# Optimization experiments

Hardware: AMD Instinct MI355X
Metric: run time of the kernel (lower is better)

## Reference

```python
import jax, jax.numpy as jnp
import numpy as np

N = 100000      # nodes
R = 3           # relations
E = 1600000     # edges per relation
IN, HID, OUT = 128, 128, 64


def setup_inputs() -> dict:
    key = jax.random.key(0)
    ks = jax.random.split(key, 16)
    x = jax.random.normal(ks[0], (N, IN), dtype=jnp.float32)
    src = jax.random.randint(ks[1], (R, E), 0, N, dtype=jnp.int32)
    dst = jax.random.randint(ks[2], (R, E), 0, N, dtype=jnp.int32)
    dims = [(IN, HID), (HID, HID), (HID, HID), (HID, HID), (HID, HID), (HID, OUT)]
    inp = {"x": x, "src": src, "dst": dst}
    for i, (di, do) in enumerate(dims):
        w = jax.random.normal(ks[3 + i], (R, di, do), dtype=jnp.float32) / np.sqrt(di).astype(np.float32)
        inp[f"W{i+1}"] = w
        inp[f"b{i+1}"] = jnp.zeros((R, do), dtype=jnp.float32)
    return inp


def _degree_norms(src, dst):
    # GraphConv norm='both': scale by out-deg(src)^-1/2 before, in-deg(dst)^-1/2 after
    ones = jnp.ones((E,), dtype=jnp.float32)
    inv_out, inv_in = [], []
    for r in range(R):
        d_out = jax.ops.segment_sum(ones, src[r], num_segments=N)
        d_in = jax.ops.segment_sum(ones, dst[r], num_segments=N)
        inv_out.append(jax.lax.rsqrt(jnp.maximum(d_out, 1.0))[:, None])
        inv_in.append(jax.lax.rsqrt(jnp.maximum(d_in, 1.0))[:, None])
    return inv_out, inv_in


def _hetero_conv(h, W, b, src, dst, inv_out, inv_in):
    # sum over relations of GraphConv_r(h): D_dst^-1/2 A_r (D_src^-1/2 h) W_r + b_r
    out = None
    for r in range(R):
        m = (h * inv_out[r]) @ W[r]                      # [N, do], weight-first (same math)
        agg = jax.ops.segment_sum(m[src[r]], dst[r], num_segments=N)
        term = agg * inv_in[r] + b[r]
        out = term if out is None else out + term
    return out


def reference(x, src, dst, W1, b1, W2, b2, W3, b3, W4, b4, W5, b5, W6, b6):
    inv_out, inv_in = _degree_norms(src, dst)
    h = x
    for W, b in [(W1, b1), (W2, b2), (W3, b3), (W4, b4), (W5, b5)]:
        h = jax.nn.relu(_hetero_conv(h, W, b, src, dst, inv_out, inv_in))
    return _hetero_conv(h, W6, b6, src, dst, inv_out, inv_in)
```

## Files before the change

kernel.cpp:

```cpp
#include <hip/hip_runtime.h>
#include <hip/hip_bf16.h>
#include <hip/hip_fp16.h>

constexpr int N_NODES = 100000;
constexpr int N_REL   = 3;
constexpr int N_EDGE  = 1600000;
constexpr int NCHUNK  = (N_NODES + 1023) / 1024;

constexpr int CCHUNK = 50;
constexpr int CH     = N_EDGE / CCHUNK;
constexpr int SUBN   = 50000;
constexpr int WPP    = SUBN / 4;
constexpr int CWORDS = N_NODES / 4;

typedef __attribute__((ext_vector_type(8))) short short8;
typedef __attribute__((ext_vector_type(4))) float f32x4;

__device__ inline ushort f2bf(float x) {
  unsigned u = __float_as_uint(x);
  unsigned r = u + 0x7FFFu + ((u >> 16) & 1u);
  return (ushort)(r >> 16);
}
__device__ inline float bf2f(ushort h) { return __uint_as_float(((unsigned)h) << 16); }


__global__ __launch_bounds__(1024)
void count_kernel(const int* __restrict__ src, const int* __restrict__ dst,
                  uint* __restrict__ part) {
  int c = blockIdx.x, r = blockIdx.y, dir = blockIdx.z;
  const int* ids = (dir ? dst : src) + (size_t)r * N_EDGE + (size_t)c * CH;
  uint* p = part + ((size_t)(c * N_REL + r) * 2 + dir) * CWORDS;
  __shared__ uint hist[WPP];
  #pragma unroll
  for (int pass = 0; pass < 2; pass++) {
    int base = pass * SUBN;
    for (int i = threadIdx.x; i < WPP; i += 1024) hist[i] = 0u;
    __syncthreads();
    for (int e = (int)threadIdx.x; e < CH; e += 1024) {
      int ln = ids[e] - base;
      if ((unsigned)ln < (unsigned)SUBN)
        atomicAdd(&hist[ln >> 2], 1u << ((ln & 3) * 8));
    }
    __syncthreads();
    for (int i = threadIdx.x; i < WPP; i += 1024) p[pass * WPP + i] = hist[i];
    __syncthreads();
  }
}

__global__ void reduce_kernel(const uint* __restrict__ part,
                              int* __restrict__ deg_out, int* __restrict__ deg_in) {
  int i = blockIdx.x * 256 + threadIdx.x;
  if (i >= N_REL * CWORDS) return;
  int r = i / CWORDS, w = i % CWORDS;
  uint aoe = 0, aoo = 0, aie = 0, aio = 0;
  for (int c = 0; c < CCHUNK; c++) {
    uint vo = part[((size_t)(c * N_REL + r) * 2 + 0) * CWORDS + w];
    uint vi = part[((size_t)(c * N_REL + r) * 2 + 1) * CWORDS + w];
    aoe += vo & 0x00FF00FFu; aoo += (vo >> 8) & 0x00FF00FFu;
    aie += vi & 0x00FF00FFu; aio += (vi >> 8) & 0x00FF00FFu;
  }
  int4 dout = make_int4((int)(aoe & 0xFFFFu), (int)(aoo & 0xFFFFu),
                        (int)(aoe >> 16),     (int)(aoo >> 16));
  int4 din  = make_int4((int)(aie & 0xFFFFu), (int)(aio & 0xFFFFu),
                        (int)(aie >> 16),     (int)(aio >> 16));
  *(int4*)&deg_out[(size_t)r * N_NODES + w * 4] = dout;
  *(int4*)&deg_in [(size_t)r * N_NODES + w * 4] = din;
}

__global__ void inv_kernel(const int* __restrict__ deg_out, const int* __restrict__ deg_in,
                           float* __restrict__ inv_out, float* __restrict__ inv_in) {
  int i = blockIdx.x * blockDim.x + threadIdx.x;
  if (i >= N_REL * N_NODES) return;
  inv_out[i] = rsqrtf(fmaxf((float)deg_out[i], 1.0f));
  inv_in[i]  = rsqrtf(fmaxf((float)deg_in[i],  1.0f));
}

__global__ void scan1_kernel(const int* __restrict__ deg_in, int* __restrict__ excl,
                             int* __restrict__ part) {
  int r = blockIdx.y;
  int i = blockIdx.x * 1024 + threadIdx.x;
  int v = (i < N_NODES) ? deg_in[r * N_NODES + i] : 0;
  __shared__ int sm[1024];
  sm[threadIdx.x] = v;
  __syncthreads();
  for (int off = 1; off < 1024; off <<= 1) {
    int t = (threadIdx.x >= (unsigned)off) ? sm[threadIdx.x - off] : 0;
    __syncthreads();
    sm[threadIdx.x] += t;
    __syncthreads();
  }
  if (i < N_NODES) excl[r * N_NODES + i] = sm[threadIdx.x] - v;
  if (threadIdx.x == 1023) part[r * NCHUNK + blockIdx.x] = sm[1023];
}

__global__ void scan2_kernel(int* __restrict__ part) {
  int r = blockIdx.x;
  int* p = part + r * NCHUNK;
  __shared__ int sm[128];
  int tid = threadIdx.x;
  int v = (tid < NCHUNK) ? p[tid] : 0;
  sm[tid] = v;
  __syncthreads();
  for (int off = 1; off < 128; off <<= 1) {
    int t = (tid >= off) ? sm[tid - off] : 0;
    __syncthreads();
    sm[tid] += t;
    __syncthreads();
  }
  if (tid < NCHUNK) p[tid] = sm[tid] - v;
}

__global__ void scan3_kernel(const int* __restrict__ excl, const int* __restrict__ part,
                             int* __restrict__ row_off) {
  int r = blockIdx.y;
  int i = blockIdx.x * 1024 + threadIdx.x;
  if (i < N_NODES) row_off[r * (N_NODES + 1) + i] = excl[r * N_NODES + i] + part[r * NCHUNK + (i >> 10)];
  if (i == N_NODES) row_off[r * (N_NODES + 1) + N_NODES] = N_EDGE;
}

__global__ void cursor_kernel(const int* __restrict__ row_off, int* __restrict__ cursor) {
  int i = blockIdx.x * 256 + threadIdx.x;
  if (i >= N_REL * N_NODES) return;
  cursor[i] = row_off[(i / N_NODES) * (N_NODES + 1) + (i % N_NODES)];
}

__global__ void scatter_kernel(const int* __restrict__ src, const int* __restrict__ dst,
                               int* __restrict__ cursor,
                               const float* __restrict__ inv_out, const float* __restrict__ inv_in,
                               float2* __restrict__ sorted_sc) {
  int tid = blockIdx.x * blockDim.x + threadIdx.x;
  if (tid >= N_REL * N_EDGE) return;
  int r = tid / N_EDGE;
  int s = src[tid], d = dst[tid];
  int o = atomicAdd(&cursor[r * N_NODES + d], 1);
  float coef = inv_out[r * N_NODES + s] * inv_in[r * N_NODES + d];
  sorted_sc[(size_t)r * N_EDGE + o] = make_float2(__int_as_float(s), coef);
}

__global__ void convw_kernel(const float* __restrict__ W, ushort* __restrict__ Wh,
                             ushort* __restrict__ Wl, int DOv) {
  int idx = blockIdx.x * 256 + threadIdx.x;
  if (idx >= 384 * DOv) return;
  int k = idx / DOv, c = idx % DOv;
  float v = W[idx];
  ushort hh = f2bf(v);
  Wh[c * 384 + k] = hh;
  Wl[c * 384 + k] = f2bf(v - bf2f(hh));
}

__global__ void convx_kernel(const float* __restrict__ x, ushort* __restrict__ x16) {
  int i = blockIdx.x * 256 + threadIdx.x;
  if (i >= N_NODES * 32) return;
  f32x4 v = ((const f32x4*)x)[i];
  __half2 h0 = __floats2half2_rn(v.x, v.y);
  __half2 h1 = __floats2half2_rn(v.z, v.w);
  uint2 o;
  o.x = *(const unsigned*)&h0;
  o.y = *(const unsigned*)&h1;
  ((uint2*)x16)[i] = o;
}


template<int P>
__device__ inline void agg_pairs(const float2* __restrict__ scp, const uint2* __restrict__ hp,
                                 int e, int sub, int l32, f32x4& acc) {
  float2 q[P];
  #pragma unroll
  for (int j = 0; j < P; j++) q[j] = scp[e + 2 * j + sub];
  uint2 v[P];
  #pragma unroll
  for (int j = 0; j < P; j++) v[j] = hp[(size_t)__float_as_int(q[j].x) * 32 + l32];
  #pragma unroll
  for (int j = 0; j < P; j++) {
    __half2 h0 = *(const __half2*)&v[j].x;
    __half2 h1 = *(const __half2*)&v[j].y;
    float2 f0 = __half22float2(h0);
    float2 f1 = __half22float2(h1);
    acc.x = fmaf(q[j].y, f0.x, acc.x);
    acc.y = fmaf(q[j].y, f0.y, acc.y);
    acc.z = fmaf(q[j].y, f1.x, acc.z);
    acc.w = fmaf(q[j].y, f1.y, acc.w);
  }
}

__launch_bounds__(256)
__global__ void agg_kernel(const ushort* __restrict__ h, const float2* __restrict__ sc,
                           const int* __restrict__ row_off,
                           ushort* __restrict__ agg_hi, ushort* __restrict__ agg_lo) {
  int r    = blockIdx.y;
  int node = blockIdx.x * 4 + ((int)threadIdx.x >> 6);
  int lane = (int)threadIdx.x & 63;
  int sub  = lane >> 5;
  int l32  = lane & 31;
  if (node >= N_NODES) return;
  const int* ro = row_off + r * (N_NODES + 1);
  int beg = ro[node], end = ro[node + 1];
  const float2* scp = sc + (size_t)r * N_EDGE;
  const uint2* hp = (const uint2*)h;
  f32x4 acc = (f32x4){0.f, 0.f, 0.f, 0.f};
  int e = beg;
  while (e + 16 <= end) { agg_pairs<8>(scp, hp, e, sub, l32, acc); e += 16; }
  if (e + 8 <= end)     { agg_pairs<4>(scp, hp, e, sub, l32, acc); e += 8; }
  if (e + 4 <= end)     { agg_pairs<2>(scp, hp, e, sub, l32, acc); e += 4; }
  if (e + 2 <= end)     { agg_pairs<1>(scp, hp, e, sub, l32, acc); e += 2; }
  if (e < end && sub == 0) {
    float2 q = scp[e];
    uint2 v = hp[(size_t)__float_as_int(q.x) * 32 + l32];
    __half2 h0 = *(const __half2*)&v.x;
    __half2 h1 = *(const __half2*)&v.y;
    float2 f0 = __half22float2(h0);
    float2 f1 = __half22float2(h1);
    acc.x = fmaf(q.y, f0.x, acc.x);
    acc.y = fmaf(q.y, f0.y, acc.y);
    acc.z = fmaf(q.y, f1.x, acc.z);
    acc.w = fmaf(q.y, f1.y, acc.w);
  }
  acc.x += __shfl_xor(acc.x, 32);
  acc.y += __shfl_xor(acc.y, 32);
  acc.z += __shfl_xor(acc.z, 32);
  acc.w += __shfl_xor(acc.w, 32);
  float a0 = (sub == 0) ? acc.x : acc.z;
  float a1 = (sub == 0) ? acc.y : acc.w;
  ushort2 hi, lo;
  hi.x = f2bf(a0); lo.x = f2bf(a0 - bf2f(hi.x));
  hi.y = f2bf(a1); lo.y = f2bf(a1 - bf2f(hi.y));
  size_t base = (size_t)node * 384 + r * 128 + l32 * 4 + sub * 2;
  *(ushort2*)(agg_hi + base) = hi;
  *(ushort2*)(agg_lo + base) = lo;
}

template<int DO, bool F16OUT>
__launch_bounds__(256)
__global__ void gemm_kernel(const ushort* __restrict__ Ah, const ushort* __restrict__ Al,
                            const ushort* __restrict__ Wh, const ushort* __restrict__ Wl,
                            const float* __restrict__ b, float* __restrict__ out,
                            ushort* __restrict__ out16, int apply_relu) {
  constexpr int K   = 384;
  constexpr int KC  = 32;
  constexpr int NCT = DO / 16;
  constexpr int LDA = 40;
  __shared__ ushort As_hi[128 * LDA], As_lo[128 * LDA];
  __shared__ ushort Bs_hi[DO * LDA],  Bs_lo[DO * LDA];
  int tid  = threadIdx.x;
  int wave = tid >> 6, lane = tid & 63;
  int quad = lane >> 4, m16 = lane & 15;
  int m0 = blockIdx.x * 128;

  f32x4 acc[2][NCT];
  #pragma unroll
  for (int rt = 0; rt < 2; rt++)
    #pragma unroll
    for (int ct = 0; ct < NCT; ct++) acc[rt][ct] = (f32x4){0.f, 0.f, 0.f, 0.f};

  for (int kc = 0; kc < K; kc += KC) {
    __syncthreads();
    #pragma unroll
    for (int it = 0; it < 2; it++) {
      int idx = it * 256 + tid;
      int row = idx >> 2, kq = (idx & 3) * 8;
      uint4 vh = make_uint4(0u, 0u, 0u, 0u), vl = make_uint4(0u, 0u, 0u, 0u);
      if (m0 + row < N_NODES) {
        vh = *(const uint4*)(Ah + (size_t)(m0 + row) * K + kc + kq);
        vl = *(const uint4*)(Al + (size_t)(m0 + row) * K + kc + kq);
      }
      *(uint4*)&As_hi[row * LDA + kq] = vh;
      *(uint4*)&As_lo[row * LDA + kq] = vl;
    }
    #pragma unroll
    for (int it = 0; it < DO / 64; it++) {
      int idx = it * 256 + tid;
      int n = idx >> 2, kq = (idx & 3) * 8;
      *(uint4*)&Bs_hi[n * LDA + kq] = *(const uint4*)(Wh + (size_t)n * K + kc + kq);
      *(uint4*)&Bs_lo[n * LDA + kq] = *(const uint4*)(Wl + (size_t)n * K + kc + kq);
    }
    __syncthreads();

    short8 ah[2], al[2];
    #pragma unroll
    for (int rt = 0; rt < 2; rt++) {
      int m = wave * 32 + rt * 16 + m16;
      ah[rt] = *(const short8*)&As_hi[m * LDA + quad * 8];
      al[rt] = *(const short8*)&As_lo[m * LDA + quad * 8];
    }
    #pragma unroll
    for (int ct = 0; ct < NCT; ct++) {
      int n = ct * 16 + m16;
      short8 bh = *(const short8*)&Bs_hi[n * LDA + quad * 8];
      short8 bl = *(const short8*)&Bs_lo[n * LDA + quad * 8];
      #pragma unroll
      for (int rt = 0; rt < 2; rt++) {
        acc[rt][ct] = __builtin_amdgcn_mfma_f32_16x16x32_bf16(ah[rt], bh, acc[rt][ct], 0, 0, 0);
        acc[rt][ct] = __builtin_amdgcn_mfma_f32_16x16x32_bf16(ah[rt], bl, acc[rt][ct], 0, 0, 0);
        acc[rt][ct] = __builtin_amdgcn_mfma_f32_16x16x32_bf16(al[rt], bh, acc[rt][ct], 0, 0, 0);
      }
    }
  }
  #pragma unroll
  for (int ct = 0; ct < NCT; ct++) {
    int col = ct * 16 + m16;
    float bs = b[col] + b[DO + col] + b[2 * DO + col];
    #pragma unroll
    for (int rt = 0; rt < 2; rt++) {
      #pragma unroll
      for (int v = 0; v < 4; v++) {
        int row = m0 + wave * 32 + rt * 16 + quad * 4 + v;
        if (row < N_NODES) {
          float o = acc[rt][ct][v] + bs;
          if (apply_relu) o = fmaxf(o, 0.f);
          if (F16OUT) {
            __half ho = __float2half_rn(o);
            out16[(size_t)row * DO + col] = *(const ushort*)&ho;
          } else {
            out[(size_t)row * DO + col] = o;
          }
        }
      }
    }
  }
}


extern "C" void kernel_launch(void* const* d_in, const int* in_sizes, int n_in,
                              void* d_out, int out_size, void* d_ws, size_t ws_size,
                              hipStream_t stream) {
  const float* x   = (const float*)d_in[0];
  const int*   src = (const int*)d_in[1];
  const int*   dst = (const int*)d_in[2];
  const float* Wl6[6]; const float* bl[6];
  for (int i = 0; i < 6; i++) { Wl6[i] = (const float*)d_in[3 + 2*i]; bl[i] = (const float*)d_in[4 + 2*i]; }

  char* ws = (char*)d_ws;
  size_t off = 0;
  auto take = [&](size_t bytes) -> char* {
    char* p = ws + off;
    off = (off + bytes + 255) & ~(size_t)255;
    return p;
  };
  ushort* h16     = (ushort*)take((size_t)N_NODES * 128 * 2);
  ushort* agg_hi  = (ushort*)take((size_t)N_NODES * 384 * 2);
  ushort* agg_lo  = (ushort*)take((size_t)N_NODES * 384 * 2);
  int*    deg     = (int*)  take((size_t)2 * N_REL * N_NODES * 4);
  int*    deg_out = deg;
  int*    deg_in  = deg + N_REL * N_NODES;
  float*  inv_out = (float*)take((size_t)N_REL * N_NODES * 4);
  float*  inv_in  = (float*)take((size_t)N_REL * N_NODES * 4);
  int*    row_off = (int*)  take((size_t)N_REL * (N_NODES + 1) * 4);
  int*    part    = (int*)  take((size_t)N_REL * NCHUNK * 4);
  float2* s_sc    = (float2*)take((size_t)N_REL * N_EDGE * 8);
  ushort* Wt      = (ushort*)take((size_t)6 * 384 * 128 * 2 * 2);
  int*    excl    = (int*)agg_hi;
  uint*   cpart   = (uint*)agg_lo;
  int*    cursor  = deg_in;
  (void)ws_size; (void)in_sizes; (void)n_in; (void)out_size;

  const int nblocks = (N_REL * N_NODES + 255) / 256;
  const int eblocks = (N_REL * N_EDGE + 255) / 256;

  count_kernel<<<dim3(CCHUNK, N_REL, 2), 1024, 0, stream>>>(src, dst, cpart);
  reduce_kernel<<<(N_REL * CWORDS + 255) / 256, 256, 0, stream>>>(cpart, deg_out, deg_in);
  inv_kernel<<<nblocks, 256, 0, stream>>>(deg_out, deg_in, inv_out, inv_in);
  scan1_kernel<<<dim3(NCHUNK, 3), 1024, 0, stream>>>(deg_in, excl, part);
  scan2_kernel<<<3, 128, 0, stream>>>(part);
  scan3_kernel<<<dim3(NCHUNK + 1, 3), 1024, 0, stream>>>(excl, part, row_off);
  cursor_kernel<<<nblocks, 256, 0, stream>>>(row_off, cursor);
  scatter_kernel<<<eblocks, 256, 0, stream>>>(src, dst, cursor, inv_out, inv_in, s_sc);

  convx_kernel<<<(N_NODES * 32 + 255) / 256, 256, 0, stream>>>(x, h16);

  ushort* Wh[6]; ushort* Wlo[6];
  {
    size_t woff = 0;
    for (int L = 0; L < 6; L++) {
      int DOv = (L < 5) ? 128 : 64;
      Wh[L]  = Wt + woff;  woff += (size_t)384 * DOv;
      Wlo[L] = Wt + woff;  woff += (size_t)384 * DOv;
      convw_kernel<<<(384 * DOv + 255) / 256, 256, 0, stream>>>(Wl6[L], Wh[L], Wlo[L], DOv);
    }
  }

  const int mtiles = (N_NODES + 127) / 128;
  const int agg_blocks = (N_NODES + 3) / 4;
  for (int L = 0; L < 6; L++) {
    agg_kernel<<<dim3(agg_blocks, 3), 256, 0, stream>>>(h16, s_sc, row_off, agg_hi, agg_lo);
    if (L < 5) {
      gemm_kernel<128, true><<<mtiles, 256, 0, stream>>>(agg_hi, agg_lo, Wh[L], Wlo[L], bl[L],
                                                         nullptr, h16, 1);
    } else {
      gemm_kernel<64, false><<<mtiles, 256, 0, stream>>>(agg_hi, agg_lo, Wh[L], Wlo[L], bl[L],
                                                         (float*)d_out, nullptr, 0);
    }
  }
}
```

Measured before the change: 1.928 ms.

## Replace per-node atomic scatter with two-pass binned counting sort

The direct scatter into CSR order, which used one global atomic per destination node, becomes a two-pass sort. The first pass bins edges into coarse 128-node buckets using global atomics, and the second pass does a per-bucket scatter with shared-memory atomics and computes the coefficients. The aim is more local writes and less random global atomic traffic during CSR build. The cost is an extra pass over the edges and a temporary buffer placed inside agg_hi.

Result: slower. 2.643 ms (+37.1%).

```diff
diff --git a/kernel.cpp b/kernel.cpp
--- a/kernel.cpp
+++ b/kernel.cpp
@@ -12,6 +12,10 @@
 constexpr int SUBN   = 50000;
 constexpr int WPP    = SUBN / 4;
 constexpr int CWORDS = N_NODES / 4;
+
+constexpr int BSH  = 7;
+constexpr int BNPB = 1 << BSH;
+constexpr int NB   = (N_NODES + BNPB - 1) / BNPB;
 
 typedef __attribute__((ext_vector_type(8))) short short8;
 typedef __attribute__((ext_vector_type(4))) float f32x4;
@@ -118,23 +122,44 @@
   if (i == N_NODES) row_off[r * (N_NODES + 1) + N_NODES] = N_EDGE;
 }
 
-__global__ void cursor_kernel(const int* __restrict__ row_off, int* __restrict__ cursor) {
-  int i = blockIdx.x * 256 + threadIdx.x;
-  if (i >= N_REL * N_NODES) return;
-  cursor[i] = row_off[(i / N_NODES) * (N_NODES + 1) + (i % N_NODES)];
-}
-
-__global__ void scatter_kernel(const int* __restrict__ src, const int* __restrict__ dst,
-                               int* __restrict__ cursor,
-                               const float* __restrict__ inv_out, const float* __restrict__ inv_in,
-                               float2* __restrict__ sorted_sc) {
+
+__global__ void bin_kernel(const int* __restrict__ src, const int* __restrict__ dst,
+                           const int* __restrict__ row_off, int* __restrict__ bcur,
+                           int2* __restrict__ binned) {
   int tid = blockIdx.x * blockDim.x + threadIdx.x;
   if (tid >= N_REL * N_EDGE) return;
   int r = tid / N_EDGE;
   int s = src[tid], d = dst[tid];
-  int o = atomicAdd(&cursor[r * N_NODES + d], 1);
-  float coef = inv_out[r * N_NODES + s] * inv_in[r * N_NODES + d];
-  sorted_sc[(size_t)r * N_EDGE + o] = make_float2(__int_as_float(s), coef);
+  int b = d >> BSH;
+  int base = row_off[r * (N_NODES + 1) + (b << BSH)];
+  int o = atomicAdd(&bcur[r * NB + b], 1);
+  binned[(size_t)r * N_EDGE + base + o] = make_int2(s, d);
+}
+
+__global__ __launch_bounds__(256)
+void scatter2_kernel(const int2* __restrict__ binned, const int* __restrict__ row_off,
+                     const float* __restrict__ inv_out, const float* __restrict__ inv_in,
+                     float2* __restrict__ sorted_sc) {
+  int b = blockIdx.x, r = blockIdx.y;
+  int node0 = b << BSH;
+  int node1 = min(node0 + BNPB, N_NODES);
+  const int* ro = row_off + r * (N_NODES + 1);
+  int base = ro[node0];
+  int m    = ro[node1] - base;
+  __shared__ int cur[BNPB];
+  for (int j = threadIdx.x; j < node1 - node0; j += 256)
+    cur[j] = ro[node0 + j] - base;
+  __syncthreads();
+  const int2* bp = binned + (size_t)r * N_EDGE + base;
+  float2* op = sorted_sc + (size_t)r * N_EDGE + base;
+  const float* ivo = inv_out + r * N_NODES;
+  const float* ivi = inv_in  + r * N_NODES;
+  for (int i = threadIdx.x; i < m; i += 256) {
+    int2 rec = bp[i];
+    int pos = atomicAdd(&cur[rec.y - node0], 1);
+    float coef = ivo[rec.x] * ivi[rec.y];
+    op[pos] = make_float2(__int_as_float(rec.x), coef);
+  }
 }
 
 __global__ void convw_kernel(const float* __restrict__ W, ushort* __restrict__ Wh,
@@ -346,11 +371,12 @@
   float*  inv_in  = (float*)take((size_t)N_REL * N_NODES * 4);
   int*    row_off = (int*)  take((size_t)N_REL * (N_NODES + 1) * 4);
   int*    part    = (int*)  take((size_t)N_REL * NCHUNK * 4);
+  int*    bcur    = (int*)  take((size_t)N_REL * NB * 4);
   float2* s_sc    = (float2*)take((size_t)N_REL * N_EDGE * 8);
   ushort* Wt      = (ushort*)take((size_t)6 * 384 * 128 * 2 * 2);
   int*    excl    = (int*)agg_hi;
+  int2*   binned  = (int2*)((char*)agg_hi + (size_t)(2 << 20));
   uint*   cpart   = (uint*)agg_lo;
-  int*    cursor  = deg_in;
   (void)ws_size; (void)in_sizes; (void)n_in; (void)out_size;
 
   const int nblocks = (N_REL * N_NODES + 255) / 256;
@@ -362,8 +388,9 @@
   scan1_kernel<<<dim3(NCHUNK, 3), 1024, 0, stream>>>(deg_in, excl, part);
   scan2_kernel<<<3, 128, 0, stream>>>(part);
   scan3_kernel<<<dim3(NCHUNK + 1, 3), 1024, 0, stream>>>(excl, part, row_off);
-  cursor_kernel<<<nblocks, 256, 0, stream>>>(row_off, cursor);
-  scatter_kernel<<<eblocks, 256, 0, stream>>>(src, dst, cursor, inv_out, inv_in, s_sc);
+  hipMemsetAsync(bcur, 0, (size_t)N_REL * NB * 4, stream);
+  bin_kernel<<<eblocks, 256, 0, stream>>>(src, dst, row_off, bcur, binned);
+  scatter2_kernel<<<dim3(NB, N_REL), 256, 0, stream>>>(binned, row_off, inv_out, inv_in, s_sc);
 
   convx_kernel<<<(N_NODES * 32 + 255) / 256, 256, 0, stream>>>(x, h16);
 
```
